# Optimization experiments

Hardware: AMD Instinct MI355X
Metric: run time of the kernel (lower is better)

Reference implementation:

```python
import jax, jax.numpy as jnp
import numpy as np

B, T, N, F_, KH, D, KD = 16, 12, 325, 64, 4, 16, 3  # batch, time, nodes, feat, heads, head_dim, diffusion steps
H = KH // 2
EPS = 1e-5


def setup_inputs() -> dict:
    key = jax.random.key(0)
    ks = jax.random.split(key, 16)
    lin = lambda k: (jax.random.normal(k, (F_, F_), jnp.float32) * 0.02)
    return {
        "x": jax.random.normal(ks[0], (B, T, N, F_), jnp.float32),
        "A": jax.random.uniform(ks[1], (KD, N, N), jnp.float32),
        "AT": jax.random.uniform(ks[2], (KD, N, N), jnp.float32),
        "Wq": lin(ks[3]), "bq": jnp.zeros((F_,), jnp.float32),
        "Wk": lin(ks[4]), "bk": jnp.zeros((F_,), jnp.float32),
        "Wks": lin(ks[5]), "bks": jnp.zeros((F_,), jnp.float32),
        "Wv": lin(ks[6]), "bv": jnp.zeros((F_,), jnp.float32),
        "Wvs": lin(ks[7]), "bvs": jnp.zeros((F_,), jnp.float32),
        "Wdi": jax.random.normal(ks[8], (H, KD, N, N), jnp.float32) * 0.05,
        "Wdo": jax.random.normal(ks[9], (H, KD, N, N), jnp.float32) * 0.05,
        "Wf1": lin(ks[10]), "bf1": jnp.zeros((F_,), jnp.float32),
        "Wf2": lin(ks[11]), "bf2": jnp.zeros((F_,), jnp.float32),
        "g_ln": jnp.ones((F_,), jnp.float32), "b_ln": jnp.zeros((F_,), jnp.float32),
    }


def _heads(y):
    # [B,T,N,F] -> [KH,B,T,N,D]  (torch.split along -1 then stack on dim 0)
    return y.reshape(B, T, N, KH, D).transpose(3, 0, 1, 2, 4)


def _attn_half(q, k, ks_, v, vs, bias):
    # q,k,ks_,v,vs: [H,B,T,N,D]; bias: [H,1,1,N,N]
    scale = 1.0 / jnp.sqrt(jnp.float32(D))
    e = jnp.einsum('hbtnd,hbtmd->hbtnm', q, k) * scale + bias
    es = jax.nn.sigmoid((q * ks_).sum(-1, keepdims=True) * scale)  # [H,B,T,N,1]
    e = e - e.max(-1, keepdims=True)
    ex = jnp.exp(e)
    a = ex / (es + ex.sum(-1, keepdims=True))  # sigmoid-augmented softmax
    out = jnp.einsum('hbtnm,hbtmd->hbtnd', a, v)
    return out + vs - a.sum(-1, keepdims=True) * vs


def reference(x, A, AT, Wq, bq, Wk, bk, Wks, bks, Wv, bv, Wvs, bvs,
              Wdi, Wdo, Wf1, bf1, Wf2, bf2, g_ln, b_ln):
    q = _heads(x @ Wq.T + bq)
    k = _heads(x @ Wk.T + bk)
    ks_ = _heads(x @ Wks.T + bks)
    v = _heads(x @ Wv.T + bv)
    vs = _heads(x @ Wvs.T + bvs)

    # DCN graph-diffusion bias: sum_j W[h,j] * A[j] -> [H,1,1,N,N]
    bias_i = jnp.einsum('hknm,knm->hnm', Wdi, A)[:, None, None]
    bias_o = jnp.einsum('hknm,knm->hnm', Wdo, AT)[:, None, None]

    vi = _attn_half(q[:H], k[:H], ks_[:H], v[:H], vs[:H], bias_i)
    vo = _attn_half(q[H:], k[H:], ks_[H:], v[H:], vs[H:], bias_o)

    val = jnp.concatenate([vi, vo], 0)  # [KH,B,T,N,D]
    val = val.transpose(1, 2, 3, 0, 4).reshape(B, T, N, F_)

    h = jax.nn.gelu(val @ Wf1.T + bf1, approximate=False) @ Wf2.T + bf2
    h = h + x

    mu = h.mean(-1, keepdims=True)
    var = ((h - mu) ** 2).mean(-1, keepdims=True)
    return g_ln * (h - mu) / jnp.sqrt(var + EPS) + b_ln
```

## Files before the change

kernel.cpp:

```cpp
#include <hip/hip_runtime.h>
#include <hip/hip_bf16.h>
#include <math.h>

#define NN 325
#define FD 64
#define KH 4
#define DH 16
#define BT 192
#define NN2 (NN*NN)
#define PST (NN*DH)
#define WSL 5632
#define HSTR 72
#define NPROJ 975
#define NPB   488
#define NBIAS 1848
#define NPAD  (KH*BT)
#define ANB   2112
#define FNB   488
#define LOG2E 1.44269504088896f

typedef __attribute__((ext_vector_type(8))) short short8;
typedef __attribute__((ext_vector_type(4))) float f32x4;

union U8 { uint4 u; short8 s; ushort us[8]; };
__device__ inline short8 lds8(const ushort* p){ U8 t; t.u = *(const uint4*)p; return t.s; }
__device__ inline float b2f(ushort v){ return __uint_as_float(((unsigned)v) << 16); }
__device__ inline ushort f2b(float f){
  unsigned u = __float_as_uint(f);
  u += 0x7fff + ((u >> 16) & 1);
  return (ushort)(u >> 16);
}
__device__ inline unsigned pk2(float a, float b){
  union { __hip_bfloat162 h; unsigned u; } t;
  t.h = __float22bfloat162_rn(float2{a, b});
  return t.u;
}
__device__ inline short8 cvt8(const float* p){
  float4 u = ((const float4*)p)[0], v = ((const float4*)p)[1];
  U8 t;
  t.us[0]=f2b(u.x); t.us[1]=f2b(u.y); t.us[2]=f2b(u.z); t.us[3]=f2b(u.w);
  t.us[4]=f2b(v.x); t.us[5]=f2b(v.y); t.us[6]=f2b(v.z); t.us[7]=f2b(v.w);
  return t.s;
}

__global__ __launch_bounds__(256) void wpack_kernel(
    const float* __restrict__ Wq,  const float* __restrict__ bq,
    const float* __restrict__ Wk,  const float* __restrict__ bk,
    const float* __restrict__ Wks, const float* __restrict__ bks,
    const float* __restrict__ Wv,  const float* __restrict__ bv,
    const float* __restrict__ Wvs, const float* __restrict__ bvs,
    const float* __restrict__ Wf1, const float* __restrict__ Wf2,
    ushort* __restrict__ Wcat, float* __restrict__ bcat){
  int blk = blockIdx.x;
  const float* Ws[7] = {Wq, Wk, Wks, Wv, Wvs, Wf1, Wf2};
  const float* bs[5] = {bq, bk, bks, bv, bvs};
  int f = blk * 64 + (threadIdx.x >> 2);
  int c0 = (threadIdx.x & 3) * 8;
  const float* wr = Ws[blk] + (f & 63) * 64;
  unsigned* dst = (unsigned*)Wcat + f * 32 + c0;
  #pragma unroll
  for (int c = 0; c < 8; ++c)
    dst[c] = f2b(wr[2*(c0+c)]) | ((unsigned)f2b(wr[2*(c0+c)+1]) << 16);
  if (blk < 5 && (threadIdx.x & 3) == 0) bcat[f] = bs[blk][f & 63];
}

__global__ __launch_bounds__(256) void prep_kernel(
    const float* __restrict__ x, const ushort* __restrict__ Wcat,
    const float* __restrict__ bcat, ushort* __restrict__ proj,
    ushort* __restrict__ vt, ushort* __restrict__ kperm,
    const float* __restrict__ Wdi, const float* __restrict__ Wdo,
    const float* __restrict__ A,   const float* __restrict__ AT,
    float* __restrict__ biasF){
  int bid = blockIdx.x, tid = threadIdx.x;
  if (bid < NPB){
    int lane = tid & 63, wid = tid >> 6;
    int m = lane & 15, g = lane >> 4;
    int gra = (bid * 64) + wid * 16 + m;
    int bta = gra / NN, na = gra - bta * NN;
    int bidB = bid + NPB;
    int bvB = (bidB < NPROJ);
    int grb = bvB ? (bidB * 64 + wid * 16 + m) : gra;
    int btb = grb / NN, nb = grb - btb * NN;

    const float* xra = x + (size_t)gra * 64 + g * 8;
    const float* xrb = x + (size_t)grb * 64 + g * 8;
    short8 xa0 = cvt8(xra), xa1 = cvt8(xra + 32);
    short8 xb0 = cvt8(xrb), xb1 = cvt8(xrb + 32);

    for (int ct = 0; ct < 20; ++ct){
      short8 w0 = lds8(Wcat + ((size_t)(ct*16 + m) * 64 + g * 8));
      short8 w1 = lds8(Wcat + ((size_t)(ct*16 + m) * 64 + g * 8 + 32));
      float4 b4 = *(const float4*)(bcat + ct*16 + 4*g);
      f32x4 bc = {b4.x, b4.y, b4.z, b4.w};
      f32x4 accA = __builtin_amdgcn_mfma_f32_16x16x32_bf16(w0, xa0, bc, 0, 0, 0);
      accA = __builtin_amdgcn_mfma_f32_16x16x32_bf16(w1, xa1, accA, 0, 0, 0);
      f32x4 accB = __builtin_amdgcn_mfma_f32_16x16x32_bf16(w0, xb0, bc, 0, 0, 0);
      accB = __builtin_amdgcn_mfma_f32_16x16x32_bf16(w1, xb1, accB, 0, 0, 0);
      if (ct >= 4 && ct < 8){
        {
          int w = na & 31;
          ushort* kd = kperm + (size_t)((ct-4)*BT + bta) * WSL
                     + (na >> 5)*512 + ((w >> 2) & 1)*256
                     + (4*(w >> 3) + (w & 3))*16 + 4*g;
          uint2 wv; wv.x = pk2(accA[0], accA[1]); wv.y = pk2(accA[2], accA[3]);
          *(uint2*)kd = wv;
        }
        if (bvB){
          int w = nb & 31;
          ushort* kd = kperm + (size_t)((ct-4)*BT + btb) * WSL
                     + (nb >> 5)*512 + ((w >> 2) & 1)*256
                     + (4*(w >> 3) + (w & 3))*16 + 4*g;
          uint2 wv; wv.x = pk2(accB[0], accB[1]); wv.y = pk2(accB[2], accB[3]);
          *(uint2*)kd = wv;
        }
      } else if (ct >= 12 && ct < 16){
        {
          ushort* vs = vt + (size_t)((ct-12)*BT + bta) * WSL + (na >> 5)*512 + (na & 31);
          #pragma unroll
          for (int rg = 0; rg < 4; ++rg)
            vs[(4*g + rg) * 32] = f2b(accA[rg]);
        }
        if (bvB){
          ushort* vs = vt + (size_t)((ct-12)*BT + btb) * WSL + (nb >> 5)*512 + (nb & 31);
          #pragma unroll
          for (int rg = 0; rg < 4; ++rg)
            vs[(4*g + rg) * 32] = f2b(accB[rg]);
        }
      } else {
        int slot = (ct < 4) ? ct : (ct < 12 ? ct - 4 : ct - 8);
        float sc = (ct < 4) ? 0.25f * LOG2E : 1.0f;
        {
          uint2 w2;
          w2.x = pk2(accA[0]*sc, accA[1]*sc);
          w2.y = pk2(accA[2]*sc, accA[3]*sc);
          *(uint2*)(proj + ((size_t)slot * BT + bta) * PST + na*16 + 4*g) = w2;
        }
        if (bvB){
          uint2 w2;
          w2.x = pk2(accB[0]*sc, accB[1]*sc);
          w2.y = pk2(accB[2]*sc, accB[3]*sc);
          *(uint2*)(proj + ((size_t)slot * BT + btb) * PST + nb*16 + 4*g) = w2;
        }
      }
    }
  } else if (bid < NPB + NBIAS){
    int idx = (bid - NPB) * 256 + tid;
    int h = idx / 118272;
    int rem = idx - h * 118272;
    int qt = rem / 5632;
    int r2 = rem - qt * 5632;
    int tt = r2 >> 9, r3 = r2 & 511;
    int gg = r3 >> 7, mm = (r3 >> 3) & 15, e8 = r3 & 7;
    int n = qt*16 + mm;
    int tok = tt*32 + gg*8 + e8;
    float s = -1e30f;
    if (n < NN && tok < NN){
      int ridx = n * NN + tok;
      s = 0.f;
      if (h < 2){
        #pragma unroll
        for (int k = 0; k < 3; ++k) s += Wdi[(h*3 + k)*NN2 + ridx] * A[k*NN2 + ridx];
      } else {
        int h2 = h - 2;
        #pragma unroll
        for (int k = 0; k < 3; ++k) s += Wdo[(h2*3 + k)*NN2 + ridx] * AT[k*NN2 + ridx];
      }
      s *= LOG2E;
    }
    biasF[idx] = s;
  } else {
    int slice = bid - NPB - NBIAS;
    if (tid < 432){
      int d = tid / 27, wz = 5 + tid % 27;
      vt[(size_t)slice * WSL + 5120 + d*32 + wz] = 0;
      int half = (wz >> 2) & 1, rr = 4*(wz >> 3) + (wz & 3);
      kperm[(size_t)slice * WSL + 5120 + half*256 + rr*16 + d] = 0;
    }
  }
}

__global__ __launch_bounds__(256, 3) void attn_kernel(
    const ushort* __restrict__ proj, const float* __restrict__ biasF,
    const ushort* __restrict__ vt, const ushort* __restrict__ kperm,
    ushort* __restrict__ val){
  int tid = threadIdx.x, lane = tid & 63, wid = tid >> 6;
  int bid = (int)blockIdx.x;
  int swz = (bid & 7) * (ANB/8) + (bid >> 3);
  int p = swz * 4 + wid;
  int j = p % 11, bh = p / 11;
  int h = bh / BT, bt = bh - h * BT;
  int qt1 = 2*j;
  int two = (j < 10);
  int qt2 = two ? qt1 + 1 : qt1;
  int m = lane & 15, g = lane >> 4;

  const ushort* qb  = proj + (size_t)((0*KH + h)*BT + bt) * PST;
  const ushort* ksb = proj + (size_t)((1*KH + h)*BT + bt) * PST;
  const ushort* vsb = proj + (size_t)((2*KH + h)*BT + bt) * PST;
  const ushort* ka  = kperm + (size_t)(h*BT + bt) * WSL + m*16 + (g&1)*8;
  const ushort* va  = vt    + (size_t)(h*BT + bt) * WSL + m*32 + g*8;
  const float*  b1a = biasF + (size_t)(h*21 + qt1) * WSL + g*128 + m*8;
  const float*  b2a = biasF + (size_t)(h*21 + qt2) * WSL + g*128 + m*8;

  short8 zero = {0,0,0,0,0,0,0,0};
  short8 qf1 = (g < 2) ? lds8(qb + (size_t)(qt1*16 + m)*16 + (g&1)*8) : zero;
  short8 qf2 = (g < 2) ? lds8(qb + (size_t)(qt2*16 + m)*16 + (g&1)*8) : zero;

  int nb1 = min(qt1*16 + m, NN-1), nb2 = min(qt2*16 + m, NN-1);
  uint2 qw1 = *(const uint2*)(qb  + (size_t)nb1*16 + g*4);
  uint2 kw1 = *(const uint2*)(ksb + (size_t)nb1*16 + g*4);
  uint2 qw2 = *(const uint2*)(qb  + (size_t)nb2*16 + g*4);
  uint2 kw2 = *(const uint2*)(ksb + (size_t)nb2*16 + g*4);

  short8 kE = lds8(ka), kO = lds8(ka + 256), vv = lds8(va);
  f32x4 bE1 = *(const f32x4*)(b1a), bO1 = *(const f32x4*)(b1a + 4);
  f32x4 bE2 = *(const f32x4*)(b2a), bO2 = *(const f32x4*)(b2a + 4);

  short8 ones = {16256,16256,16256,16256,16256,16256,16256,16256};
  f32x4 o1 = {0.f,0.f,0.f,0.f}, o2 = {0.f,0.f,0.f,0.f};
  f32x4 r1 = {0.f,0.f,0.f,0.f}, r2 = {0.f,0.f,0.f,0.f};

  #pragma unroll
  for (int tt = 0; tt < 11; ++tt){
    short8 kEn = zero, kOn = zero, vvn = zero;
    f32x4 bE1n = bE1, bO1n = bO1, bE2n = bE2, bO2n = bO2;
    if (tt < 10){
      const ushort* kan = ka + (tt+1)*512;
      kEn  = lds8(kan); kOn = lds8(kan + 256);
      vvn  = lds8(va + (tt+1)*512);
      bE1n = *(const f32x4*)(b1a + (tt+1)*512);
      bO1n = *(const f32x4*)(b1a + (tt+1)*512 + 4);
      bE2n = *(const f32x4*)(b2a + (tt+1)*512);
      bO2n = *(const f32x4*)(b2a + (tt+1)*512 + 4);
    }
    f32x4 aE1 = __builtin_amdgcn_mfma_f32_16x16x32_bf16(kE, qf1, bE1, 0, 0, 0);
    f32x4 aO1 = __builtin_amdgcn_mfma_f32_16x16x32_bf16(kO, qf1, bO1, 0, 0, 0);
    float e0 = __builtin_amdgcn_exp2f(aE1[0]);
    float e1 = __builtin_amdgcn_exp2f(aE1[1]);
    float e2 = __builtin_amdgcn_exp2f(aE1[2]);
    float e3 = __builtin_amdgcn_exp2f(aE1[3]);
    float e4 = __builtin_amdgcn_exp2f(aO1[0]);
    float e5 = __builtin_amdgcn_exp2f(aO1[1]);
    float e6 = __builtin_amdgcn_exp2f(aO1[2]);
    float e7 = __builtin_amdgcn_exp2f(aO1[3]);
    U8 p1;
    p1.u.x = pk2(e0, e1); p1.u.y = pk2(e2, e3);
    p1.u.z = pk2(e4, e5); p1.u.w = pk2(e6, e7);
    o1 = __builtin_amdgcn_mfma_f32_16x16x32_bf16(p1.s, vv,   o1, 0, 0, 0);
    r1 = __builtin_amdgcn_mfma_f32_16x16x32_bf16(p1.s, ones, r1, 0, 0, 0);
    f32x4 aE2 = __builtin_amdgcn_mfma_f32_16x16x32_bf16(kE, qf2, bE2, 0, 0, 0);
    f32x4 aO2 = __builtin_amdgcn_mfma_f32_16x16x32_bf16(kO, qf2, bO2, 0, 0, 0);
    float f0 = __builtin_amdgcn_exp2f(aE2[0]);
    float f1 = __builtin_amdgcn_exp2f(aE2[1]);
    float f2 = __builtin_amdgcn_exp2f(aE2[2]);
    float f3 = __builtin_amdgcn_exp2f(aE2[3]);
    float f4 = __builtin_amdgcn_exp2f(aO2[0]);
    float f5 = __builtin_amdgcn_exp2f(aO2[1]);
    float f6 = __builtin_amdgcn_exp2f(aO2[2]);
    float f7 = __builtin_amdgcn_exp2f(aO2[3]);
    U8 p2;
    p2.u.x = pk2(f0, f1); p2.u.y = pk2(f2, f3);
    p2.u.z = pk2(f4, f5); p2.u.w = pk2(f6, f7);
    o2 = __builtin_amdgcn_mfma_f32_16x16x32_bf16(p2.s, vv,   o2, 0, 0, 0);
    r2 = __builtin_amdgcn_mfma_f32_16x16x32_bf16(p2.s, ones, r2, 0, 0, 0);
    kE = kEn; kO = kOn; vv = vvn;
    bE1 = bE1n; bO1 = bO1n; bE2 = bE2n; bO2 = bO2n;
  }

  float dp1 = b2f((ushort)(qw1.x & 0xffff)) * b2f((ushort)(kw1.x & 0xffff))
            + b2f((ushort)(qw1.x >> 16))    * b2f((ushort)(kw1.x >> 16))
            + b2f((ushort)(qw1.y & 0xffff)) * b2f((ushort)(kw1.y & 0xffff))
            + b2f((ushort)(qw1.y >> 16))    * b2f((ushort)(kw1.y >> 16));
  float dp2 = b2f((ushort)(qw2.x & 0xffff)) * b2f((ushort)(kw2.x & 0xffff))
            + b2f((ushort)(qw2.x >> 16))    * b2f((ushort)(kw2.x >> 16))
            + b2f((ushort)(qw2.y & 0xffff)) * b2f((ushort)(kw2.y & 0xffff))
            + b2f((ushort)(qw2.y >> 16))    * b2f((ushort)(kw2.y >> 16));
  dp1 += __shfl_xor(dp1, 16, 64); dp1 += __shfl_xor(dp1, 32, 64);
  dp2 += __shfl_xor(dp2, 16, 64); dp2 += __shfl_xor(dp2, 32, 64);
  int sb = g << 4;
  #pragma unroll
  for (int rg = 0; rg < 4; ++rg){
    float d1 = __uint_as_float(__builtin_amdgcn_ds_bpermute(sb + rg*4, __float_as_uint(dp1)));
    float d2 = __uint_as_float(__builtin_amdgcn_ds_bpermute(sb + rg*4, __float_as_uint(dp2)));
    float es1 = __builtin_amdgcn_rcpf(1.f + __builtin_amdgcn_exp2f(-d1));
    float es2 = __builtin_amdgcn_rcpf(1.f + __builtin_amdgcn_exp2f(-d2));
    int n1 = qt1*16 + 4*g + rg;
    int n2 = qt2*16 + 4*g + rg;
    float vsx1 = b2f(vsb[(size_t)min(n1, NN-1)*16 + m]);
    float vsx2 = b2f(vsb[(size_t)min(n2, NN-1)*16 + m]);
    float iv1 = __builtin_amdgcn_rcpf(es1 + r1[rg]);
    float res1 = (o1[rg] + es1 * vsx1) * iv1;
    if (n1 < NN) val[((size_t)bt*NN + n1)*FD + h*16 + m] = f2b(res1);
    if (two){
      float iv2 = __builtin_amdgcn_rcpf(es2 + r2[rg]);
      float res2 = (o2[rg] + es2 * vsx2) * iv2;
      if (n2 < NN) val[((size_t)bt*NN + n2)*FD + h*16 + m] = f2b(res2);
    }
  }
}

__global__ __launch_bounds__(256) void ffn_kernel(
    const ushort* __restrict__ val, const float* __restrict__ x,
    const ushort* __restrict__ Wf1b, const float* __restrict__ bf1,
    const ushort* __restrict__ Wf2b, const float* __restrict__ bf2,
    const float* __restrict__ g_ln, const float* __restrict__ b_ln,
    float* __restrict__ out){
  __shared__ ushort hs[4][2][16 * HSTR];
  int tid = threadIdx.x, lane = tid & 63, wid = tid >> 6;
  int m = lane & 15, g = lane >> 4;
  int bid = (int)blockIdx.x;
  int rowA = bid * 64 + wid * 16 + m;
  int bidB = bid + FNB;
  int bvB = (bidB < NPROJ);
  int rowB = bvB ? (bidB * 64 + wid * 16 + m) : rowA;

  short8 va0 = lds8(val + ((size_t)rowA * 64 + g * 8));
  short8 va1 = lds8(val + ((size_t)rowA * 64 + g * 8 + 32));
  short8 vb0 = lds8(val + ((size_t)rowB * 64 + g * 8));
  short8 vb1 = lds8(val + ((size_t)rowB * 64 + g * 8 + 32));

  #pragma unroll
  for (int ct = 0; ct < 4; ++ct){
    short8 w0 = lds8(Wf1b + ((size_t)(ct*16 + m) * 64 + g * 8));
    short8 w1 = lds8(Wf1b + ((size_t)(ct*16 + m) * 64 + g * 8 + 32));
    float4 b4 = *(const float4*)(bf1 + ct*16 + 4*g);
    f32x4 bc = {b4.x, b4.y, b4.z, b4.w};
    f32x4 aA = __builtin_amdgcn_mfma_f32_16x16x32_bf16(w0, va0, bc, 0, 0, 0);
    aA = __builtin_amdgcn_mfma_f32_16x16x32_bf16(w1, va1, aA, 0, 0, 0);
    f32x4 aB = __builtin_amdgcn_mfma_f32_16x16x32_bf16(w0, vb0, bc, 0, 0, 0);
    aB = __builtin_amdgcn_mfma_f32_16x16x32_bf16(w1, vb1, aB, 0, 0, 0);
    uint2 wA, wB;
    float a0 = 0.5f*aA[0]*(1.f + erff(aA[0]*0.70710678118654752f));
    float a1 = 0.5f*aA[1]*(1.f + erff(aA[1]*0.70710678118654752f));
    float a2 = 0.5f*aA[2]*(1.f + erff(aA[2]*0.70710678118654752f));
    float a3 = 0.5f*aA[3]*(1.f + erff(aA[3]*0.70710678118654752f));
    float c0 = 0.5f*aB[0]*(1.f + erff(aB[0]*0.70710678118654752f));
    float c1 = 0.5f*aB[1]*(1.f + erff(aB[1]*0.70710678118654752f));
    float c2 = 0.5f*aB[2]*(1.f + erff(aB[2]*0.70710678118654752f));
    float c3 = 0.5f*aB[3]*(1.f + erff(aB[3]*0.70710678118654752f));
    wA.x = pk2(a0, a1); wA.y = pk2(a2, a3);
    wB.x = pk2(c0, c1); wB.y = pk2(c2, c3);
    *(uint2*)&hs[wid][0][m * HSTR + ct*16 + 4*g] = wA;
    *(uint2*)&hs[wid][1][m * HSTR + ct*16 + 4*g] = wB;
  }
  asm volatile("s_waitcnt lgkmcnt(0)" ::: "memory");
  short8 hA0 = lds8(&hs[wid][0][m * HSTR + g * 8]);
  short8 hA1 = lds8(&hs[wid][0][m * HSTR + g * 8 + 32]);
  short8 hB0 = lds8(&hs[wid][1][m * HSTR + g * 8]);
  short8 hB1 = lds8(&hs[wid][1][m * HSTR + g * 8 + 32]);

  float tA[4][4], tB[4][4];
  #pragma unroll
  for (int ct = 0; ct < 4; ++ct){
    short8 w0 = lds8(Wf2b + ((size_t)(ct*16 + m) * 64 + g * 8));
    short8 w1 = lds8(Wf2b + ((size_t)(ct*16 + m) * 64 + g * 8 + 32));
    float4 b4 = *(const float4*)(bf2 + ct*16 + 4*g);
    f32x4 bc = {b4.x, b4.y, b4.z, b4.w};
    f32x4 aA = __builtin_amdgcn_mfma_f32_16x16x32_bf16(w0, hA0, bc, 0, 0, 0);
    aA = __builtin_amdgcn_mfma_f32_16x16x32_bf16(w1, hA1, aA, 0, 0, 0);
    f32x4 aB = __builtin_amdgcn_mfma_f32_16x16x32_bf16(w0, hB0, bc, 0, 0, 0);
    aB = __builtin_amdgcn_mfma_f32_16x16x32_bf16(w1, hB1, aB, 0, 0, 0);
    float4 xrA = *(const float4*)(x + (size_t)rowA * 64 + ct*16 + 4*g);
    float4 xrB = *(const float4*)(x + (size_t)rowB * 64 + ct*16 + 4*g);
    tA[ct][0] = aA[0] + xrA.x; tA[ct][1] = aA[1] + xrA.y;
    tA[ct][2] = aA[2] + xrA.z; tA[ct][3] = aA[3] + xrA.w;
    tB[ct][0] = aB[0] + xrB.x; tB[ct][1] = aB[1] + xrB.y;
    tB[ct][2] = aB[2] + xrB.z; tB[ct][3] = aB[3] + xrB.w;
  }
  float sA = 0.f, sB = 0.f;
  #pragma unroll
  for (int ct = 0; ct < 4; ++ct){
    sA += (tA[ct][0]+tA[ct][1]) + (tA[ct][2]+tA[ct][3]);
    sB += (tB[ct][0]+tB[ct][1]) + (tB[ct][2]+tB[ct][3]);
  }
  sA += __shfl_xor(sA, 16, 64); sA += __shfl_xor(sA, 32, 64);
  sB += __shfl_xor(sB, 16, 64); sB += __shfl_xor(sB, 32, 64);
  float muA = sA * (1.f/64.f), muB = sB * (1.f/64.f);
  float vA = 0.f, vB = 0.f;
  #pragma unroll
  for (int ct = 0; ct < 4; ++ct){
    #pragma unroll
    for (int rg = 0; rg < 4; ++rg){
      float dA = tA[ct][rg] - muA; vA += dA*dA;
      float dB = tB[ct][rg] - muB; vB += dB*dB;
    }
  }
  vA += __shfl_xor(vA, 16, 64); vA += __shfl_xor(vA, 32, 64);
  vB += __shfl_xor(vB, 16, 64); vB += __shfl_xor(vB, 32, 64);
  float rsA = rsqrtf(vA * (1.f/64.f) + 1e-5f);
  float rsB = rsqrtf(vB * (1.f/64.f) + 1e-5f);
  #pragma unroll
  for (int ct = 0; ct < 4; ++ct){
    float4 g4 = *(const float4*)(g_ln + ct*16 + 4*g);
    float4 bb = *(const float4*)(b_ln + ct*16 + 4*g);
    float4 oA;
    oA.x = g4.x*(tA[ct][0]-muA)*rsA + bb.x;
    oA.y = g4.y*(tA[ct][1]-muA)*rsA + bb.y;
    oA.z = g4.z*(tA[ct][2]-muA)*rsA + bb.z;
    oA.w = g4.w*(tA[ct][3]-muA)*rsA + bb.w;
    *(float4*)(out + (size_t)rowA * 64 + ct*16 + 4*g) = oA;
    if (bvB){
      float4 oB;
      oB.x = g4.x*(tB[ct][0]-muB)*rsB + bb.x;
      oB.y = g4.y*(tB[ct][1]-muB)*rsB + bb.y;
      oB.z = g4.z*(tB[ct][2]-muB)*rsB + bb.z;
      oB.w = g4.w*(tB[ct][3]-muB)*rsB + bb.w;
      *(float4*)(out + (size_t)rowB * 64 + ct*16 + 4*g) = oB;
    }
  }
}

extern "C" void kernel_launch(void* const* d_in, const int* in_sizes, int n_in,
                              void* d_out, int out_size, void* d_ws, size_t ws_size,
                              hipStream_t stream) {
  const float* x    = (const float*)d_in[0];
  const float* A    = (const float*)d_in[1];
  const float* AT   = (const float*)d_in[2];
  const float* Wq   = (const float*)d_in[3];
  const float* bq   = (const float*)d_in[4];
  const float* Wk   = (const float*)d_in[5];
  const float* bk   = (const float*)d_in[6];
  const float* Wks  = (const float*)d_in[7];
  const float* bks  = (const float*)d_in[8];
  const float* Wv   = (const float*)d_in[9];
  const float* bv   = (const float*)d_in[10];
  const float* Wvs  = (const float*)d_in[11];
  const float* bvs  = (const float*)d_in[12];
  const float* Wdi  = (const float*)d_in[13];
  const float* Wdo  = (const float*)d_in[14];
  const float* Wf1  = (const float*)d_in[15];
  const float* bf1  = (const float*)d_in[16];
  const float* Wf2  = (const float*)d_in[17];
  const float* bf2  = (const float*)d_in[18];
  const float* g_ln = (const float*)d_in[19];
  const float* b_ln = (const float*)d_in[20];
  float* out = (float*)d_out;

  float* ws = (float*)d_ws;
  ushort* proj  = (ushort*)ws;
  float*  biasF = ws + 5990400;
  ushort* val   = (ushort*)(ws + 6463488);
  ushort* vt    = (ushort*)(ws + 8460288);
  ushort* kperm = (ushort*)(ws + 10622976);
  ushort* Wcat  = (ushort*)(ws + 12785664);
  float*  bcat  = ws + 12800000;
  ushort* Wf1b  = Wcat + 320*64;
  ushort* Wf2b  = Wcat + 384*64;

  wpack_kernel<<<7, 256, 0, stream>>>(Wq, bq, Wk, bk, Wks, bks,
                                      Wv, bv, Wvs, bvs, Wf1, Wf2, Wcat, bcat);
  prep_kernel<<<NPB + NBIAS + NPAD, 256, 0, stream>>>(
      x, Wcat, bcat, proj, vt, kperm, Wdi, Wdo, A, AT, biasF);
  attn_kernel<<<ANB, 256, 0, stream>>>(proj, biasF, vt, kperm, val);
  ffn_kernel<<<FNB, 256, 0, stream>>>(val, x, Wf1b, bf1, Wf2b, bf2,
                                      g_ln, b_ln, out);
}
```

Measured before the change: 179.4 us.

## Pre-convert x to bf16 and split projection across more blocks by weight group

The fp32-to-bf16 conversion of x moves into the weight-pack kernel, which writes a bf16 copy to the workspace. The projection stage in prep_kernel is re-split so each block handles one of five weight groups (4 column tiles) for 64 rows. Before, each block did two row tiles across all 20 column tiles. This raises the block count from 488 to 4875 for more parallelism and shorter per-block serial loops, at the cost of reading x five times (as bf16) and an extra write and read of the bf16 x buffer.

```diff
diff --git a/kernel.cpp b/kernel.cpp
--- a/kernel.cpp
+++ b/kernel.cpp
@@ -12,7 +12,7 @@
 #define WSL 5632
 #define HSTR 72
 #define NPROJ 975
-#define NPB   488
+#define NPP   4875
 #define NBIAS 1848
 #define NPAD  (KH*BT)
 #define ANB   2112
@@ -35,12 +35,12 @@
   t.h = __float22bfloat162_rn(float2{a, b});
   return t.u;
 }
-__device__ inline short8 cvt8(const float* p){
+__device__ inline uint4 cvt8u(const float* p){
   float4 u = ((const float4*)p)[0], v = ((const float4*)p)[1];
   U8 t;
   t.us[0]=f2b(u.x); t.us[1]=f2b(u.y); t.us[2]=f2b(u.z); t.us[3]=f2b(u.w);
   t.us[4]=f2b(v.x); t.us[5]=f2b(v.y); t.us[6]=f2b(v.z); t.us[7]=f2b(v.w);
-  return t.s;
+  return t.u;
 }
 
 __global__ __launch_bounds__(256) void wpack_kernel(
@@ -50,8 +50,17 @@
     const float* __restrict__ Wv,  const float* __restrict__ bv,
     const float* __restrict__ Wvs, const float* __restrict__ bvs,
     const float* __restrict__ Wf1, const float* __restrict__ Wf2,
+    const float* __restrict__ x,   ushort* __restrict__ xb,
     ushort* __restrict__ Wcat, float* __restrict__ bcat){
   int blk = blockIdx.x;
+  if (blk >= 7){
+    int base = (blk - 7) * 4096 + threadIdx.x * 16;
+    uint4 a = cvt8u(x + base);
+    uint4 b = cvt8u(x + base + 8);
+    *(uint4*)(xb + base) = a;
+    *(uint4*)(xb + base + 8) = b;
+    return;
+  }
   const float* Ws[7] = {Wq, Wk, Wks, Wv, Wvs, Wf1, Wf2};
   const float* bs[5] = {bq, bk, bks, bv, bvs};
   int f = blk * 64 + (threadIdx.x >> 2);
@@ -65,86 +74,54 @@
 }
 
 __global__ __launch_bounds__(256) void prep_kernel(
-    const float* __restrict__ x, const ushort* __restrict__ Wcat,
+    const ushort* __restrict__ xb, const ushort* __restrict__ Wcat,
     const float* __restrict__ bcat, ushort* __restrict__ proj,
     ushort* __restrict__ vt, ushort* __restrict__ kperm,
     const float* __restrict__ Wdi, const float* __restrict__ Wdo,
     const float* __restrict__ A,   const float* __restrict__ AT,
     float* __restrict__ biasF){
   int bid = blockIdx.x, tid = threadIdx.x;
-  if (bid < NPB){
+  if (bid < NPP){
+    int p = bid / 975, rb = bid - p * 975;
     int lane = tid & 63, wid = tid >> 6;
     int m = lane & 15, g = lane >> 4;
-    int gra = (bid * 64) + wid * 16 + m;
-    int bta = gra / NN, na = gra - bta * NN;
-    int bidB = bid + NPB;
-    int bvB = (bidB < NPROJ);
-    int grb = bvB ? (bidB * 64 + wid * 16 + m) : gra;
-    int btb = grb / NN, nb = grb - btb * NN;
-
-    const float* xra = x + (size_t)gra * 64 + g * 8;
-    const float* xrb = x + (size_t)grb * 64 + g * 8;
-    short8 xa0 = cvt8(xra), xa1 = cvt8(xra + 32);
-    short8 xb0 = cvt8(xrb), xb1 = cvt8(xrb + 32);
-
-    for (int ct = 0; ct < 20; ++ct){
+    int gr = rb * 64 + wid * 16 + m;
+    int bt = gr / NN, n = gr - bt * NN;
+    const ushort* xr = xb + (size_t)gr * 64 + g * 8;
+    short8 xb0 = lds8(xr);
+    short8 xb1 = lds8(xr + 32);
+    float sc = (p == 0) ? 0.25f * LOG2E : 1.0f;
+    #pragma unroll
+    for (int q = 0; q < 4; ++q){
+      int ct = p * 4 + q;
       short8 w0 = lds8(Wcat + ((size_t)(ct*16 + m) * 64 + g * 8));
       short8 w1 = lds8(Wcat + ((size_t)(ct*16 + m) * 64 + g * 8 + 32));
       float4 b4 = *(const float4*)(bcat + ct*16 + 4*g);
-      f32x4 bc = {b4.x, b4.y, b4.z, b4.w};
-      f32x4 accA = __builtin_amdgcn_mfma_f32_16x16x32_bf16(w0, xa0, bc, 0, 0, 0);
-      accA = __builtin_amdgcn_mfma_f32_16x16x32_bf16(w1, xa1, accA, 0, 0, 0);
-      f32x4 accB = __builtin_amdgcn_mfma_f32_16x16x32_bf16(w0, xb0, bc, 0, 0, 0);
-      accB = __builtin_amdgcn_mfma_f32_16x16x32_bf16(w1, xb1, accB, 0, 0, 0);
-      if (ct >= 4 && ct < 8){
-        {
-          int w = na & 31;
-          ushort* kd = kperm + (size_t)((ct-4)*BT + bta) * WSL
-                     + (na >> 5)*512 + ((w >> 2) & 1)*256
-                     + (4*(w >> 3) + (w & 3))*16 + 4*g;
-          uint2 wv; wv.x = pk2(accA[0], accA[1]); wv.y = pk2(accA[2], accA[3]);
-          *(uint2*)kd = wv;
-        }
-        if (bvB){
-          int w = nb & 31;
-          ushort* kd = kperm + (size_t)((ct-4)*BT + btb) * WSL
-                     + (nb >> 5)*512 + ((w >> 2) & 1)*256
-                     + (4*(w >> 3) + (w & 3))*16 + 4*g;
-          uint2 wv; wv.x = pk2(accB[0], accB[1]); wv.y = pk2(accB[2], accB[3]);
-          *(uint2*)kd = wv;
-        }
-      } else if (ct >= 12 && ct < 16){
-        {
-          ushort* vs = vt + (size_t)((ct-12)*BT + bta) * WSL + (na >> 5)*512 + (na & 31);
-          #pragma unroll
-          for (int rg = 0; rg < 4; ++rg)
-            vs[(4*g + rg) * 32] = f2b(accA[rg]);
-        }
-        if (bvB){
-          ushort* vs = vt + (size_t)((ct-12)*BT + btb) * WSL + (nb >> 5)*512 + (nb & 31);
-          #pragma unroll
-          for (int rg = 0; rg < 4; ++rg)
-            vs[(4*g + rg) * 32] = f2b(accB[rg]);
-        }
+      f32x4 acc = {b4.x, b4.y, b4.z, b4.w};
+      acc = __builtin_amdgcn_mfma_f32_16x16x32_bf16(w0, xb0, acc, 0, 0, 0);
+      acc = __builtin_amdgcn_mfma_f32_16x16x32_bf16(w1, xb1, acc, 0, 0, 0);
+      if (p == 1){
+        int w = n & 31;
+        ushort* kd = kperm + (size_t)(q*BT + bt) * WSL
+                   + (n >> 5)*512 + ((w >> 2) & 1)*256
+                   + (4*(w >> 3) + (w & 3))*16 + 4*g;
+        uint2 wv; wv.x = pk2(acc[0], acc[1]); wv.y = pk2(acc[2], acc[3]);
+        *(uint2*)kd = wv;
+      } else if (p == 3){
+        ushort* vs = vt + (size_t)(q*BT + bt) * WSL + (n >> 5)*512 + (n & 31);
+        #pragma unroll
+        for (int rg = 0; rg < 4; ++rg)
+          vs[(4*g + rg) * 32] = f2b(acc[rg]);
       } else {
-        int slot = (ct < 4) ? ct : (ct < 12 ? ct - 4 : ct - 8);
-        float sc = (ct < 4) ? 0.25f * LOG2E : 1.0f;
-        {
-          uint2 w2;
-          w2.x = pk2(accA[0]*sc, accA[1]*sc);
-          w2.y = pk2(accA[2]*sc, accA[3]*sc);
-          *(uint2*)(proj + ((size_t)slot * BT + bta) * PST + na*16 + 4*g) = w2;
-        }
-        if (bvB){
-          uint2 w2;
-          w2.x = pk2(accB[0]*sc, accB[1]*sc);
-          w2.y = pk2(accB[2]*sc, accB[3]*sc);
-          *(uint2*)(proj + ((size_t)slot * BT + btb) * PST + nb*16 + 4*g) = w2;
-        }
+        int slot = (p == 0) ? ct : (p == 2 ? ct - 4 : ct - 8);
+        uint2 w2;
+        w2.x = pk2(acc[0]*sc, acc[1]*sc);
+        w2.y = pk2(acc[2]*sc, acc[3]*sc);
+        *(uint2*)(proj + ((size_t)slot * BT + bt) * PST + n*16 + 4*g) = w2;
       }
     }
-  } else if (bid < NPB + NBIAS){
-    int idx = (bid - NPB) * 256 + tid;
+  } else if (bid < NPP + NBIAS){
+    int idx = (bid - NPP) * 256 + tid;
     int h = idx / 118272;
     int rem = idx - h * 118272;
     int qt = rem / 5632;
@@ -169,7 +146,7 @@
     }
     biasF[idx] = s;
   } else {
-    int slice = bid - NPB - NBIAS;
+    int slice = bid - NPP - NBIAS;
     if (tid < 432){
       int d = tid / 27, wz = 5 + tid % 27;
       vt[(size_t)slice * WSL + 5120 + d*32 + wz] = 0;
@@ -444,13 +421,14 @@
   ushort* kperm = (ushort*)(ws + 10622976);
   ushort* Wcat  = (ushort*)(ws + 12785664);
   float*  bcat  = ws + 12800000;
+  ushort* xb    = (ushort*)(ws + 12800512);
   ushort* Wf1b  = Wcat + 320*64;
   ushort* Wf2b  = Wcat + 384*64;
 
-  wpack_kernel<<<7, 256, 0, stream>>>(Wq, bq, Wk, bk, Wks, bks,
-                                      Wv, bv, Wvs, bvs, Wf1, Wf2, Wcat, bcat);
-  prep_kernel<<<NPB + NBIAS + NPAD, 256, 0, stream>>>(
-      x, Wcat, bcat, proj, vt, kperm, Wdi, Wdo, A, AT, biasF);
+  wpack_kernel<<<982, 256, 0, stream>>>(Wq, bq, Wk, bk, Wks, bks,
+                                        Wv, bv, Wvs, bvs, Wf1, Wf2, x, xb, Wcat, bcat);
+  prep_kernel<<<NPP + NBIAS + NPAD, 256, 0, stream>>>(
+      xb, Wcat, bcat, proj, vt, kperm, Wdi, Wdo, A, AT, biasF);
   attn_kernel<<<ANB, 256, 0, stream>>>(proj, biasF, vt, kperm, val);
   ffn_kernel<<<FNB, 256, 0, stream>>>(val, x, Wf1b, bf1, Wf2b, bf2,
                                       g_ln, b_ln, out);
```

After: 192.3 us. 7.2% more time.
